# Kernel optimization log

Hardware: AMD Instinct MI355X
Metric: run time of the kernel (lower is better)

Reference implementation:

```python
import jax, jax.numpy as jnp
import numpy as np

N = 50000
E = 800000
HID = 128
NH = 8
DH = HID // NH


def setup_inputs() -> dict:
    key = jax.random.key(0)
    ks = jax.random.split(key, 12)
    h = jax.random.normal(ks[0], (N, HID), dtype=jnp.float32)
    row = jnp.sort(jax.random.randint(ks[1], (E,), 0, N))
    col = jax.random.randint(ks[2], (E,), 0, N)
    s = 1.0 / np.sqrt(HID)
    Wq = jax.random.uniform(ks[3], (HID, HID), jnp.float32, -s, s)
    bq = jax.random.uniform(ks[4], (HID,), jnp.float32, -s, s)
    Wk = jax.random.uniform(ks[5], (HID, HID), jnp.float32, -s, s)
    bk = jax.random.uniform(ks[6], (HID,), jnp.float32, -s, s)
    Wv = jax.random.uniform(ks[7], (HID, HID), jnp.float32, -s, s)
    bv = jax.random.uniform(ks[8], (HID,), jnp.float32, -s, s)
    Wo = jax.random.uniform(ks[9], (HID, HID), jnp.float32, -s, s)
    bo = jax.random.uniform(ks[10], (HID,), jnp.float32, -s, s)
    return {"h": h, "row": row, "col": col, "Wq": Wq, "bq": bq,
            "Wk": Wk, "bk": bk, "Wv": Wv, "bv": bv, "Wo": Wo, "bo": bo}


def reference(h, row, col, Wq, bq, Wk, bk, Wv, bv, Wo, bo):
    n = h.shape[0]
    # projections; torch view(N, dh, nh): heads are the fastest-varying axis
    q = (h @ Wq.T + bq).reshape(n, DH, NH)
    k = (h @ Wk.T + bk).reshape(n, DH, NH)
    v = (h @ Wv.T + bv).reshape(n, DH, NH)
    # sddmm: per-edge score[e, head] = sum_d q[row_e, d, head] * k[col_e, d, head]
    scores = jnp.einsum('edh,edh->eh', q[row], k[col]) / np.sqrt(DH)
    # sparse softmax over each row's neighbors (dim=1)
    m = jax.ops.segment_max(scores, row, num_segments=n)       # [N, nh]
    e = jnp.exp(scores - m[row])                               # [E, nh]
    z = jax.ops.segment_sum(e, row, num_segments=n)            # [N, nh]
    attn = e / z[row]
    # bspmm: out[i] = sum_{j in N(i)} attn[ij] * v[j]
    out = jax.ops.segment_sum(attn[:, None, :] * v[col], row, num_segments=n)
    out = out.reshape(n, HID)
    return out @ Wo.T + bo
```

## Files before the change

kernel.cpp:

```cpp
#include <hip/hip_runtime.h>
#include <hip/hip_bf16.h>
#include <math.h>

#define HID 128
#define NH 8
#define DH 16

typedef __bf16 bf16x8 __attribute__((ext_vector_type(8)));
typedef __bf16 bf16x4 __attribute__((ext_vector_type(4)));
typedef float  f32x4  __attribute__((ext_vector_type(4)));

__global__ void prep_kernel(const int* __restrict__ row, int* __restrict__ row_ptr,
                            int N_, int E_,
                            const float* __restrict__ Wq, const float* __restrict__ Wk,
                            const float* __restrict__ Wv, const float* __restrict__ Wo,
                            const float* __restrict__ bq, const float* __restrict__ bk,
                            const float* __restrict__ bv,
                            __bf16* __restrict__ Whi, __bf16* __restrict__ Wlo,
                            float* __restrict__ bias384) {
    int idx = blockIdx.x * blockDim.x + threadIdx.x;
    if (idx < 4 * 16384) {
        int j = idx >> 14;
        int rem = idx & 16383;
        float x;
        if (j < 3) {
            const float* W = (j == 0) ? Wq : (j == 1) ? Wk : Wv;
            x = W[rem];
        } else {
            int o  = rem >> 7;
            int kp = rem & 127;
            int k  = ((kp & 15) << 3) | (kp >> 4);
            x = Wo[o * 128 + k];
        }
        __bf16 hv = (__bf16)x;
        Whi[idx] = hv;
        Wlo[idx] = (__bf16)(x - (float)hv);
    }
    if (idx <= N_) {
        int lo = 0, hi = E_;
        while (lo < hi) {
            int mid = (lo + hi) >> 1;
            if (row[mid] < idx) lo = mid + 1; else hi = mid;
        }
        row_ptr[idx] = lo;
    }
    if (idx < 384) {
        int j = idx >> 7;
        int pcol = idx & 127;
        int o = ((pcol & 15) << 3) | (pcol >> 4);
        const float* b = (j == 0) ? bq : (j == 1) ? bk : bv;
        bias384[idx] = b[o];
    }
}

__global__ __launch_bounds__(256)
void qkv_mfma_kernel(const float* __restrict__ h, int M,
                     const __bf16* __restrict__ Whi, const __bf16* __restrict__ Wlo,
                     const float* __restrict__ bias384,
                     float* __restrict__ q, __bf16* __restrict__ kv) {
    __shared__ __bf16 As2[2][64 * 128];
    int tid  = threadIdx.x;
    int wv   = tid >> 6;
    int lane = tid & 63;
    int r    = lane & 15;
    int kg   = lane >> 4;
    int m0   = blockIdx.x * 64;
    int by   = blockIdx.y;

    #pragma unroll
    for (int it = 0; it < 4; ++it) {
        int flat = it * 256 + tid;
        int row  = flat >> 4;
        int s    = flat & 15;
        int g    = s ^ (row & 7);
        int grow = m0 + row; if (grow > M - 1) grow = M - 1;
        const float* src = &h[(size_t)grow * 128 + g * 8];
        float4 x0 = *(const float4*)src;
        float4 x1 = *(const float4*)(src + 4);
        float xs[8] = {x0.x, x0.y, x0.z, x0.w, x1.x, x1.y, x1.z, x1.w};
        bf16x8 hv8, lv8;
        #pragma unroll
        for (int e = 0; e < 8; ++e) {
            __bf16 hv = (__bf16)xs[e];
            hv8[e] = hv;
            lv8[e] = (__bf16)(xs[e] - (float)hv);
        }
        *(bf16x8*)&As2[0][row * 128 + s * 8] = hv8;
        *(bf16x8*)&As2[1][row * 128 + s * 8] = lv8;
    }
    __syncthreads();

    f32x4 acc[3][4];
    #pragma unroll
    for (int cf = 0; cf < 3; ++cf)
        #pragma unroll
        for (int rf = 0; rf < 4; ++rf)
            acc[cf][rf] = (f32x4){0.f, 0.f, 0.f, 0.f};

    int wrow[3], jseg[3], pcb[3];
    #pragma unroll
    for (int cf = 0; cf < 3; ++cf) {
        int fb   = wv * 48 + cf * 16;
        int seg  = fb >> 6;
        int pcol = by * 64 + (fb & 63) + r;
        int o    = ((pcol & 15) << 3) | (pcol >> 4);
        wrow[cf] = (seg * 128 + o) * 128;
        jseg[cf] = seg;
        pcb[cf]  = pcol;
    }

    #pragma unroll
    for (int t = 0; t < 4; ++t) {
        int k0   = t * 32 + kg * 8;
        int slot = t * 4 + kg;
        bf16x8 bh[3], bl[3];
        #pragma unroll
        for (int cf = 0; cf < 3; ++cf) {
            bh[cf] = *(const bf16x8*)&Whi[wrow[cf] + k0];
            bl[cf] = *(const bf16x8*)&Wlo[wrow[cf] + k0];
        }
        bf16x8 ah[4], al[4];
        #pragma unroll
        for (int rf = 0; rf < 4; ++rf) {
            int row = rf * 16 + r;
            int s2  = slot ^ (r & 7);
            ah[rf] = *(bf16x8*)&As2[0][row * 128 + s2 * 8];
            al[rf] = *(bf16x8*)&As2[1][row * 128 + s2 * 8];
        }
        #pragma unroll
        for (int cf = 0; cf < 3; ++cf) {
            #pragma unroll
            for (int rf = 0; rf < 4; ++rf) {
                acc[cf][rf] = __builtin_amdgcn_mfma_f32_16x16x32_bf16(ah[rf], bh[cf], acc[cf][rf], 0, 0, 0);
                acc[cf][rf] = __builtin_amdgcn_mfma_f32_16x16x32_bf16(al[rf], bh[cf], acc[cf][rf], 0, 0, 0);
            }
        }
    }

    __syncthreads();
    __bf16* kvs = &As2[0][0];
    int orow = kg * 4;
    #pragma unroll
    for (int cf = 0; cf < 3; ++cf) {
        int j    = jseg[cf];
        int pcol = pcb[cf];
        float b  = bias384[j * 128 + pcol];
        #pragma unroll
        for (int rf = 0; rf < 4; ++rf) {
            #pragma unroll
            for (int e = 0; e < 4; ++e) {
                int mrow = rf * 16 + orow + e;
                float val = acc[cf][rf][e] + b;
                if (j == 0) {
                    int mg = m0 + mrow;
                    if (mg < M) q[(size_t)mg * 128 + pcol] = val;
                } else {
                    int gl  = (pcol & 63) >> 2;
                    int idx = gl * 8 + ((j == 1) ? 0 : 4) + (pcol & 3);
                    kvs[mrow * 128 + idx] = (__bf16)val;
                }
            }
        }
    }
    __syncthreads();
    #pragma unroll
    for (int it = 0; it < 4; ++it) {
        int flat = it * 256 + tid;
        int row  = flat >> 4;
        int u    = flat & 15;
        int mg   = m0 + row;
        if (mg < M)
            *(uint4*)&kv[(size_t)mg * 256 + by * 128 + u * 8] =
                *(uint4*)&kvs[row * 128 + u * 8];
    }
}

__device__ __forceinline__ float blo(unsigned u) { return __uint_as_float(u << 16); }
__device__ __forceinline__ float bhi(unsigned u) { return __uint_as_float(u & 0xffff0000u); }

__global__ __launch_bounds__(256)
void edge_attn_kernel(const int* __restrict__ row_ptr, const int* __restrict__ col,
                      const float* __restrict__ q, const __bf16* __restrict__ kv,
                      __bf16* __restrict__ obhi, __bf16* __restrict__ oblo, int N_) {
    int wave = threadIdx.x >> 6;
    int lane = threadIdx.x & 63;
    int node = blockIdx.x * 4 + wave;
    if (node >= N_) return;
    int sl   = lane & 31;
    int half = lane >> 5;

    float4 q4 = *(const float4*)&q[(size_t)node * 128 + sl * 4];
    int e0 = row_ptr[node];
    int e1 = row_ptr[node + 1];

    float m = -INFINITY, z = 0.f;
    float4 acc = make_float4(0.f, 0.f, 0.f, 0.f);

    auto score = [&](uint4 u) {
        float p = q4.x * blo(u.x) + q4.y * bhi(u.x) +
                  q4.z * blo(u.y) + q4.w * bhi(u.y);
        p += __shfl_xor(p, 1);
        p += __shfl_xor(p, 2);
        return p * 0.25f;
    };
    auto update = [&](float s, uint4 u) {
        float mnew  = fmaxf(m, s);
        float alpha = __expf(m - mnew);
        float w     = __expf(s - mnew);
        z = z * alpha + w;
        acc.x = acc.x * alpha + w * blo(u.z);
        acc.y = acc.y * alpha + w * bhi(u.z);
        acc.z = acc.z * alpha + w * blo(u.w);
        acc.w = acc.w * alpha + w * bhi(u.w);
        m = mnew;
    };

    int eb = e0;
    for (; eb + 4 <= e1; eb += 4) {
        int ea = eb + half * 2;
        int c0 = col[ea];
        int c1 = col[ea + 1];
        uint4 u0 = *(const uint4*)(kv + (size_t)c0 * 256 + sl * 8);
        uint4 u1 = *(const uint4*)(kv + (size_t)c1 * 256 + sl * 8);
        float s0 = score(u0);
        float s1 = score(u1);
        update(s0, u0);
        update(s1, u1);
    }
    for (; eb < e1; eb += 2) {
        int my_e   = eb + half;
        bool valid = (my_e < e1);
        int cnode  = valid ? col[my_e] : col[eb];
        uint4 u = *(const uint4*)(kv + (size_t)cnode * 256 + sl * 8);
        float s = valid ? score(u) : -INFINITY;
        float mnew = fmaxf(m, s);
        if (mnew > -INFINITY) {
            float alpha = __expf(m - mnew);
            float w     = __expf(s - mnew);
            z = z * alpha + w;
            acc.x = acc.x * alpha + w * blo(u.z);
            acc.y = acc.y * alpha + w * bhi(u.z);
            acc.z = acc.z * alpha + w * blo(u.w);
            acc.w = acc.w * alpha + w * bhi(u.w);
            m = mnew;
        }
    }

    float m2 = __shfl_xor(m, 32);
    float z2 = __shfl_xor(z, 32);
    float ax = __shfl_xor(acc.x, 32);
    float ay = __shfl_xor(acc.y, 32);
    float az = __shfl_xor(acc.z, 32);
    float aw = __shfl_xor(acc.w, 32);
    float mm = fmaxf(m, m2);
    if (mm > -INFINITY) {
        float a1 = __expf(m - mm);
        float a2 = __expf(m2 - mm);
        z = z * a1 + z2 * a2;
        acc.x = acc.x * a1 + ax * a2;
        acc.y = acc.y * a1 + ay * a2;
        acc.z = acc.z * a1 + az * a2;
        acc.w = acc.w * a1 + aw * a2;
    }

    if (half == 0) {
        float inv = (z > 0.f) ? 1.0f / z : 0.f;
        float rr[4] = {acc.x * inv, acc.y * inv, acc.z * inv, acc.w * inv};
        bf16x4 hv4, lv4;
        #pragma unroll
        for (int jj = 0; jj < 4; ++jj) {
            __bf16 hv = (__bf16)rr[jj];
            hv4[jj] = hv;
            lv4[jj] = (__bf16)(rr[jj] - (float)hv);
        }
        *(bf16x4*)&obhi[(size_t)node * 128 + sl * 4] = hv4;
        *(bf16x4*)&oblo[(size_t)node * 128 + sl * 4] = lv4;
    }
}

__global__ __launch_bounds__(256)
void outproj_mfma_kernel(const __bf16* __restrict__ Ahi_g, const __bf16* __restrict__ Alo_g,
                         int M, const __bf16* __restrict__ Whi, const __bf16* __restrict__ Wlo,
                         const float* __restrict__ bo, float* __restrict__ C) {
    __shared__ __bf16 As2[2][64 * 128];
    int tid  = threadIdx.x;
    int wv   = tid >> 6;
    int lane = tid & 63;
    int r    = lane & 15;
    int kg   = lane >> 4;
    int m0   = blockIdx.x * 64;
    int by   = blockIdx.y;
    int col  = by * 64 + wv * 16 + r;

    #pragma unroll
    for (int it = 0; it < 4; ++it) {
        int flat = it * 256 + tid;
        int row  = flat >> 4;
        int s    = flat & 15;
        int g    = s ^ (row & 7);
        int grow = m0 + row; if (grow > M - 1) grow = M - 1;
        *(bf16x8*)&As2[0][row * 128 + s * 8] = *(const bf16x8*)&Ahi_g[(size_t)grow * 128 + g * 8];
        *(bf16x8*)&As2[1][row * 128 + s * 8] = *(const bf16x8*)&Alo_g[(size_t)grow * 128 + g * 8];
    }
    __syncthreads();

    f32x4 acc[4];
    #pragma unroll
    for (int rf = 0; rf < 4; ++rf) acc[rf] = (f32x4){0.f, 0.f, 0.f, 0.f};

    int wrow = col * 128;
    #pragma unroll
    for (int t = 0; t < 4; ++t) {
        int k0   = t * 32 + kg * 8;
        int slot = t * 4 + kg;
        bf16x8 bh = *(const bf16x8*)&Whi[wrow + k0];
        bf16x8 bl = *(const bf16x8*)&Wlo[wrow + k0];
        bf16x8 ah[4], al[4];
        #pragma unroll
        for (int rf = 0; rf < 4; ++rf) {
            int row = rf * 16 + r;
            int s2  = slot ^ (r & 7);
            ah[rf] = *(bf16x8*)&As2[0][row * 128 + s2 * 8];
            al[rf] = *(bf16x8*)&As2[1][row * 128 + s2 * 8];
        }
        #pragma unroll
        for (int rf = 0; rf < 4; ++rf) {
            acc[rf] = __builtin_amdgcn_mfma_f32_16x16x32_bf16(ah[rf], bh, acc[rf], 0, 0, 0);
            acc[rf] = __builtin_amdgcn_mfma_f32_16x16x32_bf16(al[rf], bh, acc[rf], 0, 0, 0);
        }
    }

    float b = bo[col];
    #pragma unroll
    for (int rf = 0; rf < 4; ++rf) {
        #pragma unroll
        for (int e = 0; e < 4; ++e) {
            int mg = m0 + rf * 16 + kg * 4 + e;
            if (mg < M) C[(size_t)mg * 128 + col] = acc[rf][e] + b;
        }
    }
}

extern "C" void kernel_launch(void* const* d_in, const int* in_sizes, int n_in,
                              void* d_out, int out_size, void* d_ws, size_t ws_size,
                              hipStream_t stream) {
    const float* h  = (const float*)d_in[0];
    const int* row  = (const int*)d_in[1];
    const int* col  = (const int*)d_in[2];
    const float* Wq = (const float*)d_in[3];
    const float* bq = (const float*)d_in[4];
    const float* Wk = (const float*)d_in[5];
    const float* bk = (const float*)d_in[6];
    const float* Wv = (const float*)d_in[7];
    const float* bv = (const float*)d_in[8];
    const float* Wo = (const float*)d_in[9];
    const float* bo = (const float*)d_in[10];
    float* out = (float*)d_out;

    int N_ = in_sizes[0] / HID;
    int E_ = in_sizes[1];

    char* ws = (char*)d_ws;
    size_t off = 0;
    auto alloc = [&](size_t bytes) {
        void* p = (void*)(ws + off);
        off = (off + bytes + 255) & ~(size_t)255;
        return p;
    };
    int*    row_ptr = (int*)   alloc((size_t)(N_ + 1) * sizeof(int));
    float*  qb      = (float*) alloc((size_t)N_ * 128 * sizeof(float));
    __bf16* kvb     = (__bf16*)alloc((size_t)N_ * 256 * sizeof(__bf16));
    __bf16* obhi    = (__bf16*)alloc((size_t)N_ * 128 * sizeof(__bf16));
    __bf16* oblo    = (__bf16*)alloc((size_t)N_ * 128 * sizeof(__bf16));
    __bf16* Whi     = (__bf16*)alloc((size_t)4 * 16384 * sizeof(__bf16));
    __bf16* Wlo     = (__bf16*)alloc((size_t)4 * 16384 * sizeof(__bf16));
    float*  bias384 = (float*) alloc(384 * sizeof(float));
    (void)ws_size;

    prep_kernel<<<256, 256, 0, stream>>>(row, row_ptr, N_, E_,
                                         Wq, Wk, Wv, Wo, bq, bk, bv,
                                         Whi, Wlo, bias384);
    qkv_mfma_kernel<<<dim3((N_ + 63) / 64, 2), 256, 0, stream>>>(
        h, N_, Whi, Wlo, bias384, qb, kvb);
    edge_attn_kernel<<<(N_ + 3) / 4, 256, 0, stream>>>(row_ptr, col, qb, kvb, obhi, oblo, N_);
    outproj_mfma_kernel<<<dim3((N_ + 63) / 64, 2), 256, 0, stream>>>(
        obhi, oblo, N_, Whi + 3 * 16384, Wlo + 3 * 16384, bo, out);
}
```

Measured before the change: 204.8 us.

## Drop split-bf16 compensation, store q in bf16, batch 4 edges per softmax step

Removes the hi/lo bf16 split used to emulate higher precision in both projection GEMMs, which halves the MFMA count and the A-tile shared memory and drops the Wlo weight arrays. The q buffer and the attention output are stored as single bf16 instead of fp32 or hi/lo pairs, cutting memory traffic in the edge kernel and the out-projection. The edge loop now processes 4 edges per half-wave with one block-level online-softmax rescale, giving more loads in flight and fewer exps. The cost is lower numerical accuracy throughout, which may exceed the tolerance.

```diff
diff --git a/kernel.cpp b/kernel.cpp
--- a/kernel.cpp
+++ b/kernel.cpp
@@ -16,8 +16,7 @@
                             const float* __restrict__ Wv, const float* __restrict__ Wo,
                             const float* __restrict__ bq, const float* __restrict__ bk,
                             const float* __restrict__ bv,
-                            __bf16* __restrict__ Whi, __bf16* __restrict__ Wlo,
-                            float* __restrict__ bias384) {
+                            __bf16* __restrict__ Whi, float* __restrict__ bias384) {
     int idx = blockIdx.x * blockDim.x + threadIdx.x;
     if (idx < 4 * 16384) {
         int j = idx >> 14;
@@ -32,9 +31,7 @@
             int k  = ((kp & 15) << 3) | (kp >> 4);
             x = Wo[o * 128 + k];
         }
-        __bf16 hv = (__bf16)x;
-        Whi[idx] = hv;
-        Wlo[idx] = (__bf16)(x - (float)hv);
+        Whi[idx] = (__bf16)x;
     }
     if (idx <= N_) {
         int lo = 0, hi = E_;
@@ -55,10 +52,10 @@
 
 __global__ __launch_bounds__(256)
 void qkv_mfma_kernel(const float* __restrict__ h, int M,
-                     const __bf16* __restrict__ Whi, const __bf16* __restrict__ Wlo,
+                     const __bf16* __restrict__ Whi,
                      const float* __restrict__ bias384,
-                     float* __restrict__ q, __bf16* __restrict__ kv) {
-    __shared__ __bf16 As2[2][64 * 128];
+                     __bf16* __restrict__ q, __bf16* __restrict__ kv) {
+    __shared__ __bf16 As[64 * 128];
     int tid  = threadIdx.x;
     int wv   = tid >> 6;
     int lane = tid & 63;
@@ -78,15 +75,10 @@
         float4 x0 = *(const float4*)src;
         float4 x1 = *(const float4*)(src + 4);
         float xs[8] = {x0.x, x0.y, x0.z, x0.w, x1.x, x1.y, x1.z, x1.w};
-        bf16x8 hv8, lv8;
-        #pragma unroll
-        for (int e = 0; e < 8; ++e) {
-            __bf16 hv = (__bf16)xs[e];
-            hv8[e] = hv;
-            lv8[e] = (__bf16)(xs[e] - (float)hv);
-        }
-        *(bf16x8*)&As2[0][row * 128 + s * 8] = hv8;
-        *(bf16x8*)&As2[1][row * 128 + s * 8] = lv8;
+        bf16x8 hv8;
+        #pragma unroll
+        for (int e = 0; e < 8; ++e) hv8[e] = (__bf16)xs[e];
+        *(bf16x8*)&As[row * 128 + s * 8] = hv8;
     }
     __syncthreads();
 
@@ -113,32 +105,26 @@
     for (int t = 0; t < 4; ++t) {
         int k0   = t * 32 + kg * 8;
         int slot = t * 4 + kg;
-        bf16x8 bh[3], bl[3];
-        #pragma unroll
-        for (int cf = 0; cf < 3; ++cf) {
+        bf16x8 bh[3];
+        #pragma unroll
+        for (int cf = 0; cf < 3; ++cf)
             bh[cf] = *(const bf16x8*)&Whi[wrow[cf] + k0];
-            bl[cf] = *(const bf16x8*)&Wlo[wrow[cf] + k0];
-        }
-        bf16x8 ah[4], al[4];
+        bf16x8 ah[4];
         #pragma unroll
         for (int rf = 0; rf < 4; ++rf) {
             int row = rf * 16 + r;
             int s2  = slot ^ (r & 7);
-            ah[rf] = *(bf16x8*)&As2[0][row * 128 + s2 * 8];
-            al[rf] = *(bf16x8*)&As2[1][row * 128 + s2 * 8];
-        }
-        #pragma unroll
-        for (int cf = 0; cf < 3; ++cf) {
+            ah[rf] = *(bf16x8*)&As[row * 128 + s2 * 8];
+        }
+        #pragma unroll
+        for (int cf = 0; cf < 3; ++cf)
             #pragma unroll
-            for (int rf = 0; rf < 4; ++rf) {
+            for (int rf = 0; rf < 4; ++rf)
                 acc[cf][rf] = __builtin_amdgcn_mfma_f32_16x16x32_bf16(ah[rf], bh[cf], acc[cf][rf], 0, 0, 0);
-                acc[cf][rf] = __builtin_amdgcn_mfma_f32_16x16x32_bf16(al[rf], bh[cf], acc[cf][rf], 0, 0, 0);
-            }
-        }
     }
 
     __syncthreads();
-    __bf16* kvs = &As2[0][0];
+    __bf16* kvs = &As[0];
     int orow = kg * 4;
     #pragma unroll
     for (int cf = 0; cf < 3; ++cf) {
@@ -153,7 +139,7 @@
                 float val = acc[cf][rf][e] + b;
                 if (j == 0) {
                     int mg = m0 + mrow;
-                    if (mg < M) q[(size_t)mg * 128 + pcol] = val;
+                    if (mg < M) q[(size_t)mg * 128 + pcol] = (__bf16)val;
                 } else {
                     int gl  = (pcol & 63) >> 2;
                     int idx = gl * 8 + ((j == 1) ? 0 : 4) + (pcol & 3);
@@ -180,8 +166,8 @@
 
 __global__ __launch_bounds__(256)
 void edge_attn_kernel(const int* __restrict__ row_ptr, const int* __restrict__ col,
-                      const float* __restrict__ q, const __bf16* __restrict__ kv,
-                      __bf16* __restrict__ obhi, __bf16* __restrict__ oblo, int N_) {
+                      const __bf16* __restrict__ q, const __bf16* __restrict__ kv,
+                      __bf16* __restrict__ ob, int N_) {
     int wave = threadIdx.x >> 6;
     int lane = threadIdx.x & 63;
     int node = blockIdx.x * 4 + wave;
@@ -189,7 +175,9 @@
     int sl   = lane & 31;
     int half = lane >> 5;
 
-    float4 q4 = *(const float4*)&q[(size_t)node * 128 + sl * 4];
+    uint2 qu = *(const uint2*)&q[(size_t)node * 128 + sl * 4];
+    float qx = blo(qu.x), qy = bhi(qu.x), qz = blo(qu.y), qw = bhi(qu.y);
+
     int e0 = row_ptr[node];
     int e1 = row_ptr[node + 1];
 
@@ -197,35 +185,39 @@
     float4 acc = make_float4(0.f, 0.f, 0.f, 0.f);
 
     auto score = [&](uint4 u) {
-        float p = q4.x * blo(u.x) + q4.y * bhi(u.x) +
-                  q4.z * blo(u.y) + q4.w * bhi(u.y);
+        float p = qx * blo(u.x) + qy * bhi(u.x) +
+                  qz * blo(u.y) + qw * bhi(u.y);
         p += __shfl_xor(p, 1);
         p += __shfl_xor(p, 2);
         return p * 0.25f;
     };
-    auto update = [&](float s, uint4 u) {
-        float mnew  = fmaxf(m, s);
-        float alpha = __expf(m - mnew);
-        float w     = __expf(s - mnew);
-        z = z * alpha + w;
-        acc.x = acc.x * alpha + w * blo(u.z);
-        acc.y = acc.y * alpha + w * bhi(u.z);
-        acc.z = acc.z * alpha + w * blo(u.w);
-        acc.w = acc.w * alpha + w * bhi(u.w);
-        m = mnew;
-    };
 
     int eb = e0;
-    for (; eb + 4 <= e1; eb += 4) {
-        int ea = eb + half * 2;
-        int c0 = col[ea];
-        int c1 = col[ea + 1];
+    for (; eb + 8 <= e1; eb += 8) {
+        int ea = eb + half * 4;
+        int c0 = col[ea], c1 = col[ea + 1], c2 = col[ea + 2], c3 = col[ea + 3];
         uint4 u0 = *(const uint4*)(kv + (size_t)c0 * 256 + sl * 8);
         uint4 u1 = *(const uint4*)(kv + (size_t)c1 * 256 + sl * 8);
-        float s0 = score(u0);
-        float s1 = score(u1);
-        update(s0, u0);
-        update(s1, u1);
+        uint4 u2 = *(const uint4*)(kv + (size_t)c2 * 256 + sl * 8);
+        uint4 u3 = *(const uint4*)(kv + (size_t)c3 * 256 + sl * 8);
+        float s0 = score(u0), s1 = score(u1), s2 = score(u2), s3 = score(u3);
+        float m03 = fmaxf(fmaxf(s0, s1), fmaxf(s2, s3));
+        float w0 = __expf(s0 - m03), w1 = __expf(s1 - m03);
+        float w2 = __expf(s2 - m03), w3 = __expf(s3 - m03);
+        float zl = (w0 + w1) + (w2 + w3);
+        float lx = w0 * blo(u0.z) + w1 * blo(u1.z) + w2 * blo(u2.z) + w3 * blo(u3.z);
+        float ly = w0 * bhi(u0.z) + w1 * bhi(u1.z) + w2 * bhi(u2.z) + w3 * bhi(u3.z);
+        float lz = w0 * blo(u0.w) + w1 * blo(u1.w) + w2 * blo(u2.w) + w3 * blo(u3.w);
+        float lw = w0 * bhi(u0.w) + w1 * bhi(u1.w) + w2 * bhi(u2.w) + w3 * bhi(u3.w);
+        float mn = fmaxf(m, m03);
+        float a1 = __expf(m - mn);
+        float a2 = __expf(m03 - mn);
+        z = z * a1 + zl * a2;
+        acc.x = acc.x * a1 + lx * a2;
+        acc.y = acc.y * a1 + ly * a2;
+        acc.z = acc.z * a1 + lz * a2;
+        acc.w = acc.w * a1 + lw * a2;
+        m = mn;
     }
     for (; eb < e1; eb += 2) {
         int my_e   = eb + half;
@@ -265,24 +257,20 @@
 
     if (half == 0) {
         float inv = (z > 0.f) ? 1.0f / z : 0.f;
-        float rr[4] = {acc.x * inv, acc.y * inv, acc.z * inv, acc.w * inv};
-        bf16x4 hv4, lv4;
-        #pragma unroll
-        for (int jj = 0; jj < 4; ++jj) {
-            __bf16 hv = (__bf16)rr[jj];
-            hv4[jj] = hv;
-            lv4[jj] = (__bf16)(rr[jj] - (float)hv);
-        }
-        *(bf16x4*)&obhi[(size_t)node * 128 + sl * 4] = hv4;
-        *(bf16x4*)&oblo[(size_t)node * 128 + sl * 4] = lv4;
+        bf16x4 hv4;
+        hv4[0] = (__bf16)(acc.x * inv);
+        hv4[1] = (__bf16)(acc.y * inv);
+        hv4[2] = (__bf16)(acc.z * inv);
+        hv4[3] = (__bf16)(acc.w * inv);
+        *(bf16x4*)&ob[(size_t)node * 128 + sl * 4] = hv4;
     }
 }
 
 __global__ __launch_bounds__(256)
-void outproj_mfma_kernel(const __bf16* __restrict__ Ahi_g, const __bf16* __restrict__ Alo_g,
-                         int M, const __bf16* __restrict__ Whi, const __bf16* __restrict__ Wlo,
+void outproj_mfma_kernel(const __bf16* __restrict__ A_g, int M,
+                         const __bf16* __restrict__ Whi,
                          const float* __restrict__ bo, float* __restrict__ C) {
-    __shared__ __bf16 As2[2][64 * 128];
+    __shared__ __bf16 As[64 * 128];
     int tid  = threadIdx.x;
     int wv   = tid >> 6;
     int lane = tid & 63;
@@ -299,8 +287,7 @@
         int s    = flat & 15;
         int g    = s ^ (row & 7);
         int grow = m0 + row; if (grow > M - 1) grow = M - 1;
-        *(bf16x8*)&As2[0][row * 128 + s * 8] = *(const bf16x8*)&Ahi_g[(size_t)grow * 128 + g * 8];
-        *(bf16x8*)&As2[1][row * 128 + s * 8] = *(const bf16x8*)&Alo_g[(size_t)grow * 128 + g * 8];
+        *(bf16x8*)&As[row * 128 + s * 8] = *(const bf16x8*)&A_g[(size_t)grow * 128 + g * 8];
     }
     __syncthreads();
 
@@ -314,20 +301,16 @@
         int k0   = t * 32 + kg * 8;
         int slot = t * 4 + kg;
         bf16x8 bh = *(const bf16x8*)&Whi[wrow + k0];
-        bf16x8 bl = *(const bf16x8*)&Wlo[wrow + k0];
-        bf16x8 ah[4], al[4];
+        bf16x8 ah[4];
         #pragma unroll
         for (int rf = 0; rf < 4; ++rf) {
             int row = rf * 16 + r;
             int s2  = slot ^ (r & 7);
-            ah[rf] = *(bf16x8*)&As2[0][row * 128 + s2 * 8];
-            al[rf] = *(bf16x8*)&As2[1][row * 128 + s2 * 8];
-        }
-        #pragma unroll
-        for (int rf = 0; rf < 4; ++rf) {
+            ah[rf] = *(bf16x8*)&As[row * 128 + s2 * 8];
+        }
+        #pragma unroll
+        for (int rf = 0; rf < 4; ++rf)
             acc[rf] = __builtin_amdgcn_mfma_f32_16x16x32_bf16(ah[rf], bh, acc[rf], 0, 0, 0);
-            acc[rf] = __builtin_amdgcn_mfma_f32_16x16x32_bf16(al[rf], bh, acc[rf], 0, 0, 0);
-        }
     }
 
     float b = bo[col];
@@ -368,21 +351,19 @@
         return p;
     };
     int*    row_ptr = (int*)   alloc((size_t)(N_ + 1) * sizeof(int));
-    float*  qb      = (float*) alloc((size_t)N_ * 128 * sizeof(float));
+    __bf16* qb      = (__bf16*)alloc((size_t)N_ * 128 * sizeof(__bf16));
     __bf16* kvb     = (__bf16*)alloc((size_t)N_ * 256 * sizeof(__bf16));
-    __bf16* obhi    = (__bf16*)alloc((size_t)N_ * 128 * sizeof(__bf16));
-    __bf16* oblo    = (__bf16*)alloc((size_t)N_ * 128 * sizeof(__bf16));
+    __bf16* obb     = (__bf16*)alloc((size_t)N_ * 128 * sizeof(__bf16));
     __bf16* Whi     = (__bf16*)alloc((size_t)4 * 16384 * sizeof(__bf16));
-    __bf16* Wlo     = (__bf16*)alloc((size_t)4 * 16384 * sizeof(__bf16));
     float*  bias384 = (float*) alloc(384 * sizeof(float));
     (void)ws_size;
 
     prep_kernel<<<256, 256, 0, stream>>>(row, row_ptr, N_, E_,
                                          Wq, Wk, Wv, Wo, bq, bk, bv,
-                                         Whi, Wlo, bias384);
+                                         Whi, bias384);
     qkv_mfma_kernel<<<dim3((N_ + 63) / 64, 2), 256, 0, stream>>>(
-        h, N_, Whi, Wlo, bias384, qb, kvb);
-    edge_attn_kernel<<<(N_ + 3) / 4, 256, 0, stream>>>(row_ptr, col, qb, kvb, obhi, oblo, N_);
+        h, N_, Whi, bias384, qb, kvb);
+    edge_attn_kernel<<<(N_ + 3) / 4, 256, 0, stream>>>(row_ptr, col, qb, kvb, obb, N_);
     outproj_mfma_kernel<<<dim3((N_ + 63) / 64, 2), 256, 0, stream>>>(
-        obhi, oblo, N_, Whi + 3 * 16384, Wlo + 3 * 16384, bo, out);
-}
+        obb, N_, Whi + 3 * 16384, bo, out);
+}
```

New measurement: 192.2 us. 1.07x faster.
